# Optimization experiments

Measured on AMD Instinct MI355X. Metric: run time of the kernel, lower is better.

The kernel has to match this reference:

```python
import jax, jax.numpy as jnp
import numpy as np

N, E = 25000, 400000
HID, EDGE_F, DIM, HEADS, ADY = 128, 16, 3, 8, 64
INNER = int(1.25 * HID)          # 160
MSG_F = 2 * HID + EDGE_F + 1     # 273 (e3, relaxed=False -> 1 distance feature)


def silu(x):
    return x * jax.nn.sigmoid(x)


def ada_ln(x, y, W, b):
    # LayerNorm (no affine) + FiLM conditioning from y
    mu = jnp.mean(x, axis=-1, keepdims=True)
    var = jnp.var(x, axis=-1, keepdims=True)
    xn = (x - mu) * jax.lax.rsqrt(var + 1e-5)
    scale, shift = jnp.split(y @ W + b, 2, axis=-1)
    return xn * (1.0 + scale) + shift


def setup_inputs() -> dict:
    key = jax.random.key(0)
    ks = jax.random.split(key, 32)
    rn = lambda k, shp, s=0.05: (jax.random.normal(k, shp, jnp.float32) * s)
    inp = {
        'h': jax.random.normal(ks[0], (N, HID), jnp.float32),
        'coords': jax.random.normal(ks[1], (N, DIM), jnp.float32),
        'a': jax.random.normal(ks[2], (E, EDGE_F), jnp.float32),
        'y': jax.random.normal(ks[3], (N, ADY), jnp.float32),
        'res': jnp.zeros((N, HID), jnp.float32),
        'src': jax.random.randint(ks[4], (E,), 0, N, jnp.int32),
        'dst': jax.random.randint(ks[5], (E,), 0, N, jnp.int32),
        # edge MLP
        'We1': rn(ks[6], (MSG_F, INNER)), 'be1': jnp.zeros((INNER,), jnp.float32),
        'We2': rn(ks[7], (INNER, INNER)), 'be2': jnp.zeros((INNER,), jnp.float32),
        # coord head (xavier gain 0.001 -> tiny init)
        'Wc': rn(ks[8], (INNER, 1), 0.001),
        # attention/value/output heads
        'Wv': rn(ks[9], (INNER, HID)),
        'Wa': rn(ks[10], (INNER, HEADS)),
        'Wo': rn(ks[11], (HID, HID)),
        # node MLP
        'Wn1': rn(ks[12], (HID, INNER)), 'bn1': jnp.zeros((INNER,), jnp.float32),
        'Wn2': rn(ks[13], (INNER, HID)), 'bn2': jnp.zeros((HID,), jnp.float32),
        # adaptive LayerNorms (FiLM from y)
        'Wf1': rn(ks[14], (ADY, 2 * HID)), 'bf1': jnp.zeros((2 * HID,), jnp.float32),
        'Wf2': rn(ks[15], (ADY, 2 * HID)), 'bf2': jnp.zeros((2 * HID,), jnp.float32),
    }
    return inp


def reference(h, coords, a, y, res, src, dst,
              We1, be1, We2, be2, Wc, Wv, Wa, Wo,
              Wn1, bn1, Wn2, bn2, Wf1, bf1, Wf2, bf2):
    n = h.shape[0]
    heads = Wa.shape[1]
    # --- distance features (e3, relaxed=False): radial only ---
    xs, xd = coords[src], coords[dst]          # [E, 3]
    diffs = xs - xd
    radials = jnp.sum(diffs * diffs, axis=-1, keepdims=True)  # [E, 1]
    # --- edge MLP on gathered features ---
    f = jnp.concatenate([h[src], h[dst], radials, a], axis=-1)  # [E, 273]
    m = silu(f @ We1 + be1)
    m = silu(m @ We2 + be2)                    # [E, inner]
    # --- coordinate messages + scatter-sum to dst ---
    msg_x = (m @ Wc) * diffs / (jnp.sqrt(radials + 1e-5) + 1.0)  # [E, 3]
    coords_out = coords + jax.ops.segment_sum(msg_x, dst, num_segments=n)
    # --- edge softmax over incoming edges per dst node ---
    logits = m @ Wa                             # [E, heads]
    mx = jax.ops.segment_max(logits, dst, num_segments=n)
    ex = jnp.exp(logits - mx[dst])
    den = jax.ops.segment_sum(ex, dst, num_segments=n)
    w = ex / den[dst]                           # [E, heads]
    # --- weighted value aggregation ---
    vals = (m @ Wv).reshape(-1, heads, HID // heads) * w[:, :, None]
    h_agg = jax.ops.segment_sum(vals, dst, num_segments=n).reshape(n, HID)
    f2 = h_agg @ Wo
    res1 = res + f2
    h1 = ada_ln(h + f2, y, Wf1, bf1)
    f3 = silu(h1 @ Wn1 + bn1) @ Wn2 + bn2
    res2 = res1 + f3
    h2 = ada_ln(h1 + f3, y, Wf2, bf2)
    return (h2, coords_out, res2)
```

## Files before the change

kernel.cpp:

```cpp
#include <hip/hip_runtime.h>
#include <math.h>

#define N_NODES 25000
#define N_EDGES 400000
#define HID 128
#define EDGE_F 16
#define ADY 64
#define INNER 160
#define MSG_F 273
#define HEADS 8

#define OUT_CRD (N_NODES * HID)
#define OUT_RES (N_NODES * (HID + 3))

#define FLAG_OFF 0
#define DEN_OFF  256
#define CACC_OFF 800256
#define HAGG_OFF 1100288
#define HBF_OFF  13900288
#define YBF_OFF  20300288
#define BIAS_OFF 23500288
#define BW_OFF   23502592
#define MEMSET_BYTES 13900288

typedef unsigned short u16;
typedef unsigned int u32;
typedef unsigned long long u64;
typedef __attribute__((ext_vector_type(8))) short short8;
typedef __attribute__((ext_vector_type(4))) float f32x4;

__device__ __forceinline__ float bf2f(u16 v) {
    union { u32 u; float f; } x; x.u = ((u32)v) << 16; return x.f;
}
__device__ __forceinline__ u16 f2bf(float f) {
    union { float ff; u32 u; } x; x.ff = f;
    u32 u = x.u;
    u32 rounding = 0x7FFFu + ((u >> 16) & 1u);
    u += rounding;
    return (u16)(u >> 16);
}
__device__ __forceinline__ float silu(float z) {
    z = fminf(fmaxf(z, -30000.f), 30000.f);
    return z / (1.0f + __expf(-z));
}

template<bool F32> __device__ __forceinline__ float ldg1(const void* p, size_t i) {
    if (F32) return ((const float*)p)[i];
    return bf2f(((const u16*)p)[i]);
}
template<bool F32> __device__ __forceinline__ void stg1(void* p, size_t i, float v) {
    if (F32) ((float*)p)[i] = v;
    else     ((u16*)p)[i] = f2bf(v);
}
__device__ __forceinline__ float ldany(const void* p, size_t i, bool f32) {
    return f32 ? ((const float*)p)[i] : bf2f(((const u16*)p)[i]);
}
__device__ __forceinline__ void wave_lds_fence() {
    __builtin_amdgcn_wave_barrier();
    __builtin_amdgcn_s_waitcnt(0xc07f);
    __builtin_amdgcn_wave_barrier();
}

struct CvtArgs {
    const void* src[8];
    u64 dstoff[8];
    int n[8];
};
struct BwArgs {
    const void* We1; const void* We2; const void* Wv; const void* Wa;
    const void* Wc;  const void* Wo;  const void* Wn1; const void* Wn2;
    const void* Wf1; const void* Wf2;
    u64 b1, b2, b3, b4, b5, b6, b7, b8;
};

__global__ __launch_bounds__(256)
void preproc_kernel(const void* hsrc, int* flag, char* ws, CvtArgs args, BwArgs bwa)
{
    __shared__ float red[256];
    __shared__ int sflag;
    const int t = threadIdx.x;
    {
        const u16* p = (const u16*)hsrc;
        float mx = 0.f;
        for (int i = 0; i < 8; i++) {
            int idx = (t * 8 + i) * 97;
            float v = fabsf(bf2f(p[idx * 2]));
            mx = fmaxf(mx, v);
        }
        red[t] = mx;
        __syncthreads();
        for (int s = 128; s > 0; s >>= 1) {
            if (t < s) red[t] = fmaxf(red[t], red[t + s]);
            __syncthreads();
        }
        if (t == 0) {
            sflag = (red[0] > 1e10f || red[0] == 0.f) ? 1 : 0;
            if (blockIdx.x == 0) flag[0] = sflag;
        }
        __syncthreads();
    }
    const bool f32 = (sflag != 0);
    const int g = blockIdx.x * 256 + t;
    const int stride = gridDim.x * 256;

    for (int ten = 0; ten < 8; ten++) {
        const void* s = args.src[ten];
        u16* d = (u16*)(ws + args.dstoff[ten]);
        const int n = args.n[ten];
        if (f32) {
            const float* sf = (const float*)s;
            for (int i = g; i < n; i += stride) d[i] = f2bf(sf[i]);
        } else {
            const u16* su = (const u16*)s;
            for (int i = g; i < n; i += stride) d[i] = su[i];
        }
    }

    u16* b1 = (u16*)(ws + bwa.b1);
    u16* b2 = (u16*)(ws + bwa.b2);
    u16* b3 = (u16*)(ws + bwa.b3);
    u16* b4 = (u16*)(ws + bwa.b4);
    u16* b5 = (u16*)(ws + bwa.b5);
    u16* b6 = (u16*)(ws + bwa.b6);
    u16* b7 = (u16*)(ws + bwa.b7);
    u16* b8 = (u16*)(ws + bwa.b8);
    for (int i = g; i < 5*2*10*512; i += stride) {
        int tt = i >> 9, r = i & 511, l = r >> 3, j = r & 7;
        int c = tt / 20, ks = (tt / 10) % 2, nt = tt % 10;
        int k = c*64 + ks*32 + (l >> 4)*8 + j;
        int n = nt*16 + (l & 15);
        float v = 0.f;
        if (k < MSG_F)      v = ldany(bwa.We1, (size_t)k*INNER + n, f32);
        else if (k == 273)  v = ldany(bwa.We1, (size_t)256*INNER + n, f32);
        b1[i] = f2bf(v);
    }
    for (int i = g; i < 5*10*512; i += stride) {
        int tt = i >> 9, r = i & 511, l = r >> 3, j = r & 7;
        int k5 = tt / 10, nt = tt % 10;
        int k = k5*32 + (l >> 4)*8 + j;
        int n = nt*16 + (l & 15);
        b2[i] = f2bf(ldany(bwa.We2, (size_t)k*INNER + n, f32));
    }
    for (int i = g; i < 5*9*512; i += stride) {
        int tt = i >> 9, r = i & 511, l = r >> 3, j = r & 7;
        int k5 = tt / 9, nt = tt % 9;
        int k = k5*32 + (l >> 4)*8 + j;
        int n = nt*16 + (l & 15);
        float v = 0.f;
        if (n < 128)       v = ldany(bwa.Wv, (size_t)k*HID + n, f32);
        else if (n < 136)  v = ldany(bwa.Wa, (size_t)k*HEADS + (n-128), f32);
        else if (n == 136) v = ldany(bwa.Wc, (size_t)k, f32);
        b3[i] = f2bf(v);
    }
    for (int i = g; i < 4*8*512; i += stride) {
        int tt = i >> 9, r = i & 511, l = r >> 3, j = r & 7;
        int cks = tt / 8, nt = tt % 8;
        int k = cks*32 + (l >> 4)*8 + j;
        int n = nt*16 + (l & 15);
        b4[i] = f2bf(ldany(bwa.Wo, (size_t)k*HID + n, f32));
    }
    for (int i = g; i < 4*10*512; i += stride) {
        int tt = i >> 9, r = i & 511, l = r >> 3, j = r & 7;
        int cks = tt / 10, nt = tt % 10;
        int k = cks*32 + (l >> 4)*8 + j;
        int n = nt*16 + (l & 15);
        b5[i] = f2bf(ldany(bwa.Wn1, (size_t)k*INNER + n, f32));
    }
    for (int i = g; i < 5*8*512; i += stride) {
        int tt = i >> 9, r = i & 511, l = r >> 3, j = r & 7;
        int k5 = tt / 8, nt = tt % 8;
        int k = k5*32 + (l >> 4)*8 + j;
        int n = nt*16 + (l & 15);
        b6[i] = f2bf(ldany(bwa.Wn2, (size_t)k*HID + n, f32));
    }
    for (int i = g; i < 2*16*512; i += stride) {
        int tt = i >> 9, r = i & 511, l = r >> 3, j = r & 7;
        int ks = tt / 16, nt = tt % 16;
        int k = ks*32 + (l >> 4)*8 + j;
        int n = nt*16 + (l & 15);
        b7[i] = f2bf(ldany(bwa.Wf1, (size_t)k*256 + n, f32));
        b8[i] = f2bf(ldany(bwa.Wf2, (size_t)k*256 + n, f32));
    }
}

template<bool F32>
__device__ __forceinline__ void edge_body(
    const u16* __restrict__ hbf, const void* coords, const void* a,
    const int* __restrict__ src, const int* __restrict__ dst,
    const u16* __restrict__ We1P, const u16* __restrict__ We2P,
    const u16* __restrict__ W3P,
    const u16* __restrict__ cbe1, const u16* __restrict__ cbe2,
    float* __restrict__ den, float* __restrict__ hagg, float* __restrict__ cacc,
    u16* sPool, float* sdiff, float* srad, int* ssrc, int* sdstl)
{
    const int t   = threadIdx.x;
    const int w   = t >> 6;
    const int l   = t & 63;
    const int col = l & 15;
    const int q   = l >> 4;
    const int e0  = blockIdx.x * 64;
    const int l8  = l << 3;

    u16* sF  = sPool;
    u16* sM1 = sPool;
    u16* sM2 = sPool + 64*168;

    if (t < 64) {
        int e = e0 + t;
        int s = src[e], d = dst[e];
        ssrc[t] = s; sdstl[t] = d;
        float dx = ldg1<F32>(coords, (size_t)s*3+0) - ldg1<F32>(coords, (size_t)d*3+0);
        float dy = ldg1<F32>(coords, (size_t)s*3+1) - ldg1<F32>(coords, (size_t)d*3+1);
        float dz = ldg1<F32>(coords, (size_t)s*3+2) - ldg1<F32>(coords, (size_t)d*3+2);
        sdiff[t*4+0] = dx; sdiff[t*4+1] = dy; sdiff[t*4+2] = dz;
        float r2 = dx*dx + dy*dy + dz*dz;
        srad[t] = r2;
        sdiff[t*4+3] = 1.0f / (sqrtf(r2 + 1e-5f) + 1.0f);
    }
    __syncthreads();

    {
        int e = t >> 2, part = t & 3;
        int node_s = ssrc[e], node_d = sdstl[e];
        #pragma unroll
        for (int c = 0; c < 4; c++) {
            int node = (c < 2) ? node_s : node_d;
            int c0 = (c & 1) * 64 + part * 16;
            const uint4* gp = (const uint4*)(hbf + (size_t)node*HID + c0);
            *(uint4*)(&sF[e*360 + c*72 + part*16])     = gp[0];
            *(uint4*)(&sF[e*360 + c*72 + part*16 + 8]) = gp[1];
        }
        if (part < 2) {
            __align__(16) u16 tmp[16];
            #pragma unroll
            for (int j = 0; j < 16; j++) tmp[j] = 0;
            if (part == 0) {
                float r2 = srad[e];
                tmp[0] = f2bf(r2);
                for (int j = 0; j < 15; j++)
                    tmp[1+j] = f2bf(ldg1<F32>(a, (size_t)(e0+e)*EDGE_F + j));
            } else {
                tmp[0] = f2bf(ldg1<F32>(a, (size_t)(e0+e)*EDGE_F + 15));
                float r2 = srad[e];
                tmp[1] = f2bf(r2 - bf2f(f2bf(r2)));
            }
            *(uint4*)(&sF[e*360 + 4*72 + part*16])     = ((uint4*)tmp)[0];
            *(uint4*)(&sF[e*360 + 4*72 + part*16 + 8]) = ((uint4*)tmp)[1];
        }
    }
    __syncthreads();

    f32x4 acc1[10];
    #pragma unroll
    for (int nt = 0; nt < 10; nt++) {
        float v = bf2f(cbe1[nt*16 + col]);
        acc1[nt] = (f32x4){v, v, v, v};
    }
    const u16* fbase = &sF[(w*16 + col)*360];
    #pragma unroll
    for (int c = 0; c < 4; c++) {
        #pragma unroll
        for (int ks = 0; ks < 2; ks++) {
            short8 af = *(const short8*)(fbase + c*72 + ks*32 + q*8);
            const u16* B1 = We1P + (((c*2 + ks)*10) << 9) + l8;
            #pragma unroll
            for (int nt = 0; nt < 10; nt++) {
                short8 b = *(const short8*)(B1 + (nt << 9));
                acc1[nt] = __builtin_amdgcn_mfma_f32_16x16x32_bf16(af, b, acc1[nt], 0, 0, 0);
            }
        }
    }
    {
        short8 af = *(const short8*)(fbase + 4*72 + q*8);
        const u16* B1 = We1P + ((8*10) << 9) + l8;
        #pragma unroll
        for (int nt = 0; nt < 10; nt++) {
            short8 b = *(const short8*)(B1 + (nt << 9));
            acc1[nt] = __builtin_amdgcn_mfma_f32_16x16x32_bf16(af, b, acc1[nt], 0, 0, 0);
        }
    }
    __syncthreads();
    #pragma unroll
    for (int nt = 0; nt < 10; nt++)
        #pragma unroll
        for (int r = 0; r < 4; r++)
            sM1[(w*16 + q*4 + r)*168 + nt*16 + col] = f2bf(silu(acc1[nt][r]));
    __syncthreads();

    f32x4 acc2[10];
    #pragma unroll
    for (int nt = 0; nt < 10; nt++) {
        float v = bf2f(cbe2[nt*16 + col]);
        acc2[nt] = (f32x4){v, v, v, v};
    }
    const u16* m1base = &sM1[(w*16 + col)*168];
    #pragma unroll
    for (int k5 = 0; k5 < 5; k5++) {
        short8 af = *(const short8*)(m1base + k5*32 + q*8);
        const u16* B2 = We2P + ((k5*10) << 9) + l8;
        #pragma unroll
        for (int nt = 0; nt < 10; nt++) {
            short8 b = *(const short8*)(B2 + (nt << 9));
            acc2[nt] = __builtin_amdgcn_mfma_f32_16x16x32_bf16(af, b, acc2[nt], 0, 0, 0);
        }
    }
    #pragma unroll
    for (int nt = 0; nt < 10; nt++)
        #pragma unroll
        for (int r = 0; r < 4; r++)
            sM2[(w*16 + q*4 + r)*168 + nt*16 + col] = f2bf(silu(acc2[nt][r]));
    __syncthreads();

    f32x4 acc3[9];
    #pragma unroll
    for (int nt = 0; nt < 9; nt++) acc3[nt] = (f32x4){0.f, 0.f, 0.f, 0.f};
    const u16* m2base = &sM2[(w*16 + col)*168];
    #pragma unroll
    for (int k5 = 0; k5 < 5; k5++) {
        short8 af = *(const short8*)(m2base + k5*32 + q*8);
        const u16* B3 = W3P + ((k5*9) << 9) + l8;
        #pragma unroll
        for (int nt = 0; nt < 9; nt++) {
            short8 b = *(const short8*)(B3 + (nt << 9));
            acc3[nt] = __builtin_amdgcn_mfma_f32_16x16x32_bf16(af, b, acc3[nt], 0, 0, 0);
        }
    }

    int dstep[4];
    #pragma unroll
    for (int r = 0; r < 4; r++) dstep[r] = sdstl[w*16 + q*4 + r];

    float exv[4] = {0.f, 0.f, 0.f, 0.f};
    if (col < 8) {
        #pragma unroll
        for (int r = 0; r < 4; r++) {
            float ex = __expf(fminf(fmaxf(acc3[8][r], -30.f), 30.f));
            exv[r] = ex;
            atomicAdd(&den[(size_t)dstep[r]*8 + col], ex);
        }
    } else if (col == 8) {
        #pragma unroll
        for (int r = 0; r < 4; r++) {
            int idx = w*16 + q*4 + r;
            int dd = dstep[r];
            float invf = sdiff[idx*4 + 3];
            float lc = fminf(fmaxf(acc3[8][r], -1e6f), 1e6f) * invf;
            #pragma unroll
            for (int j = 0; j < 3; j++)
                atomicAdd(&cacc[(size_t)dd*3 + j], lc * sdiff[idx*4 + j]);
        }
    }
    #pragma unroll
    for (int nt = 0; nt < 8; nt++) {
        float ex0 = __shfl(exv[0], q*16 + nt);
        float ex1 = __shfl(exv[1], q*16 + nt);
        float ex2 = __shfl(exv[2], q*16 + nt);
        float ex3 = __shfl(exv[3], q*16 + nt);
        atomicAdd(&hagg[(size_t)dstep[0]*HID + nt*16 + col], acc3[nt][0] * ex0);
        atomicAdd(&hagg[(size_t)dstep[1]*HID + nt*16 + col], acc3[nt][1] * ex1);
        atomicAdd(&hagg[(size_t)dstep[2]*HID + nt*16 + col], acc3[nt][2] * ex2);
        atomicAdd(&hagg[(size_t)dstep[3]*HID + nt*16 + col], acc3[nt][3] * ex3);
    }
}

__global__ __launch_bounds__(256, 3)
void edge_kernel(const int* __restrict__ flag,
                 const u16* __restrict__ hbf, const void* coords, const void* a,
                 const int* __restrict__ src, const int* __restrict__ dst,
                 const u16* __restrict__ We1P, const u16* __restrict__ We2P,
                 const u16* __restrict__ W3P,
                 const u16* __restrict__ cbe1, const u16* __restrict__ cbe2,
                 float* __restrict__ den, float* __restrict__ hagg,
                 float* __restrict__ cacc)
{
    __shared__ __align__(16) u16 sPool[64*360];
    __shared__ float sdiff[64*4];
    __shared__ float srad[64];
    __shared__ int   ssrc[64];
    __shared__ int   sdstl[64];
    if (*flag)
        edge_body<true>(hbf, coords, a, src, dst, We1P, We2P, W3P, cbe1, cbe2,
                        den, hagg, cacc, sPool, sdiff, srad, ssrc, sdstl);
    else
        edge_body<false>(hbf, coords, a, src, dst, We1P, We2P, W3P, cbe1, cbe2,
                         den, hagg, cacc, sPool, sdiff, srad, ssrc, sdstl);
}

template<bool F32>
__device__ __forceinline__ void node_body(
    const u16* __restrict__ hbf, const void* res, const void* coords,
    const u16* __restrict__ ybf,
    const float* __restrict__ den, const float* __restrict__ hagg,
    const float* __restrict__ cacc,
    const u16* __restrict__ WoP, const u16* __restrict__ Wn1P,
    const u16* __restrict__ Wn2P, const u16* __restrict__ Wf1P,
    const u16* __restrict__ Wf2P,
    const u16* __restrict__ cbn1, const u16* __restrict__ cbn2,
    const u16* __restrict__ cbf1, const u16* __restrict__ cbf2,
    void* out, u16* sScr)
{
    const int t = threadIdx.x;
    const int w = t >> 6, l = t & 63, col = l & 15, q = l >> 4;
    const int nodew = blockIdx.x * 64 + w * 16;
    const int mynode = nodew + col;
    const bool okA = mynode < N_NODES;
    const int l8 = l << 3;
    u16* sc = sScr + w * 16 * 168;

    int gm[4]; bool okC[4];
    #pragma unroll
    for (int r = 0; r < 4; r++) { gm[r] = nodew + q*4 + r; okC[r] = gm[r] < N_NODES; }

    f32x4 aF2[8];
    #pragma unroll
    for (int nt = 0; nt < 8; nt++) aF2[nt] = (f32x4){0.f,0.f,0.f,0.f};
    #pragma unroll
    for (int c = 0; c < 2; c++) {
        #pragma unroll
        for (int ks = 0; ks < 2; ks++) {
            const int kbase = c*64 + ks*32 + q*8;
            union { u16 s[8]; short8 v; } u;
            if (okA) {
                float dd = den[(size_t)mynode*8 + (kbase >> 4)];
                float inv = dd > 0.f ? 1.f/dd : 0.f;
                const float4* gp = (const float4*)(hagg + (size_t)mynode*HID + kbase);
                float4 v0 = gp[0], v1 = gp[1];
                u.s[0]=f2bf(v0.x*inv); u.s[1]=f2bf(v0.y*inv); u.s[2]=f2bf(v0.z*inv); u.s[3]=f2bf(v0.w*inv);
                u.s[4]=f2bf(v1.x*inv); u.s[5]=f2bf(v1.y*inv); u.s[6]=f2bf(v1.z*inv); u.s[7]=f2bf(v1.w*inv);
            } else {
                #pragma unroll
                for (int j = 0; j < 8; j++) u.s[j] = 0;
            }
            const u16* B = WoP + (((c*2 + ks)*8) << 9) + l8;
            #pragma unroll
            for (int nt = 0; nt < 8; nt++) {
                short8 b = *(const short8*)(B + (nt << 9));
                aF2[nt] = __builtin_amdgcn_mfma_f32_16x16x32_bf16(u.v, b, aF2[nt], 0, 0, 0);
            }
        }
    }

    f32x4 aFl[16];
    #pragma unroll
    for (int nt = 0; nt < 16; nt++) {
        float v = bf2f(cbf1[nt*16 + col]);
        aFl[nt] = (f32x4){v,v,v,v};
    }
    #pragma unroll
    for (int ks = 0; ks < 2; ks++) {
        short8 af;
        if (okA) af = *(const short8*)(ybf + (size_t)mynode*ADY + ks*32 + q*8);
        else { union { u16 s[8]; short8 v; } z; for (int j=0;j<8;j++) z.s[j]=0; af = z.v; }
        const u16* B = Wf1P + ((ks*16) << 9) + l8;
        #pragma unroll
        for (int nt = 0; nt < 16; nt++) {
            short8 b = *(const short8*)(B + (nt << 9));
            aFl[nt] = __builtin_amdgcn_mfma_f32_16x16x32_bf16(af, b, aFl[nt], 0, 0, 0);
        }
    }

    float h1c[8][4], r1c[8][4];
    {
        float xv[8][4], s[4], ss[4];
        #pragma unroll
        for (int r = 0; r < 4; r++) { s[r] = 0.f; ss[r] = 0.f; }
        #pragma unroll
        for (int nt = 0; nt < 8; nt++)
            #pragma unroll
            for (int r = 0; r < 4; r++) {
                float hv = okC[r] ? bf2f(hbf[(size_t)gm[r]*HID + nt*16 + col]) : 0.f;
                float x = hv + aF2[nt][r];
                xv[nt][r] = x; s[r] += x; ss[r] += x*x;
            }
        #pragma unroll
        for (int r = 0; r < 4; r++)
            for (int off = 1; off <= 8; off <<= 1) {
                s[r]  += __shfl_xor(s[r], off);
                ss[r] += __shfl_xor(ss[r], off);
            }
        #pragma unroll
        for (int r = 0; r < 4; r++) {
            float mu = s[r] * (1.f/128.f);
            float var = ss[r] * (1.f/128.f) - mu*mu;
            float rs = rsqrtf(fmaxf(var, 0.f) + 1e-5f);
            #pragma unroll
            for (int nt = 0; nt < 8; nt++) {
                float h1 = (xv[nt][r]-mu)*rs*(1.f+aFl[nt][r]) + aFl[nt+8][r];
                h1c[nt][r] = h1;
                float rv = okC[r] ? ldg1<F32>(res, (size_t)gm[r]*HID + nt*16 + col) : 0.f;
                r1c[nt][r] = rv + aF2[nt][r];
                sc[(q*4 + r)*168 + nt*16 + col] = f2bf(h1);
            }
        }
    }
    wave_lds_fence();

    f32x4 aT[10];
    #pragma unroll
    for (int nt = 0; nt < 10; nt++) {
        float v = bf2f(cbn1[nt*16 + col]);
        aT[nt] = (f32x4){v,v,v,v};
    }
    #pragma unroll
    for (int c = 0; c < 2; c++) {
        #pragma unroll
        for (int ks = 0; ks < 2; ks++) {
            short8 af = *(const short8*)(sc + col*168 + c*64 + ks*32 + q*8);
            const u16* B = Wn1P + (((c*2 + ks)*10) << 9) + l8;
            #pragma unroll
            for (int nt = 0; nt < 10; nt++) {
                short8 b = *(const short8*)(B + (nt << 9));
                aT[nt] = __builtin_amdgcn_mfma_f32_16x16x32_bf16(af, b, aT[nt], 0, 0, 0);
            }
        }
    }
    wave_lds_fence();
    #pragma unroll
    for (int nt = 0; nt < 10; nt++)
        #pragma unroll
        for (int r = 0; r < 4; r++)
            sc[(q*4 + r)*168 + nt*16 + col] = f2bf(silu(aT[nt][r]));
    wave_lds_fence();

    f32x4 aF3[8];
    #pragma unroll
    for (int nt = 0; nt < 8; nt++) {
        float v = bf2f(cbn2[nt*16 + col]);
        aF3[nt] = (f32x4){v,v,v,v};
    }
    #pragma unroll
    for (int k5 = 0; k5 < 5; k5++) {
        short8 af = *(const short8*)(sc + col*168 + k5*32 + q*8);
        const u16* B = Wn2P + ((k5*8) << 9) + l8;
        #pragma unroll
        for (int nt = 0; nt < 8; nt++) {
            short8 b = *(const short8*)(B + (nt << 9));
            aF3[nt] = __builtin_amdgcn_mfma_f32_16x16x32_bf16(af, b, aF3[nt], 0, 0, 0);
        }
    }

    #pragma unroll
    for (int nt = 0; nt < 16; nt++) {
        float v = bf2f(cbf2[nt*16 + col]);
        aFl[nt] = (f32x4){v,v,v,v};
    }
    #pragma unroll
    for (int ks = 0; ks < 2; ks++) {
        short8 af;
        if (okA) af = *(const short8*)(ybf + (size_t)mynode*ADY + ks*32 + q*8);
        else { union { u16 s[8]; short8 v; } z; for (int j=0;j<8;j++) z.s[j]=0; af = z.v; }
        const u16* B = Wf2P + ((ks*16) << 9) + l8;
        #pragma unroll
        for (int nt = 0; nt < 16; nt++) {
            short8 b = *(const short8*)(B + (nt << 9));
            aFl[nt] = __builtin_amdgcn_mfma_f32_16x16x32_bf16(af, b, aFl[nt], 0, 0, 0);
        }
    }

    {
        float xv[8][4], s[4], ss[4];
        #pragma unroll
        for (int r = 0; r < 4; r++) { s[r] = 0.f; ss[r] = 0.f; }
        #pragma unroll
        for (int nt = 0; nt < 8; nt++)
            #pragma unroll
            for (int r = 0; r < 4; r++) {
                float x = h1c[nt][r] + aF3[nt][r];
                xv[nt][r] = x; s[r] += x; ss[r] += x*x;
            }
        #pragma unroll
        for (int r = 0; r < 4; r++)
            for (int off = 1; off <= 8; off <<= 1) {
                s[r]  += __shfl_xor(s[r], off);
                ss[r] += __shfl_xor(ss[r], off);
            }
        #pragma unroll
        for (int r = 0; r < 4; r++) {
            float mu = s[r] * (1.f/128.f);
            float var = ss[r] * (1.f/128.f) - mu*mu;
            float rs = rsqrtf(fmaxf(var, 0.f) + 1e-5f);
            if (okC[r]) {
                #pragma unroll
                for (int nt = 0; nt < 8; nt++) {
                    int n = nt*16 + col;
                    float h2 = (xv[nt][r]-mu)*rs*(1.f+aFl[nt][r]) + aFl[nt+8][r];
                    stg1<F32>(out, (size_t)gm[r]*HID + n, h2);
                    stg1<F32>(out, (size_t)OUT_RES + (size_t)gm[r]*HID + n,
                              r1c[nt][r] + aF3[nt][r]);
                }
            }
        }
    }

    if (q == 0 && okA) {
        #pragma unroll
        for (int j = 0; j < 3; j++)
            stg1<F32>(out, (size_t)OUT_CRD + (size_t)mynode*3 + j,
                      ldg1<F32>(coords, (size_t)mynode*3 + j) + cacc[(size_t)mynode*3 + j]);
    }
}

__global__ __launch_bounds__(256, 2)
void node_kernel(const int* __restrict__ flag,
                 const u16* __restrict__ hbf, const void* res, const void* coords,
                 const u16* __restrict__ ybf,
                 const float* __restrict__ den, const float* __restrict__ hagg,
                 const float* __restrict__ cacc,
                 const u16* __restrict__ WoP, const u16* __restrict__ Wn1P,
                 const u16* __restrict__ Wn2P, const u16* __restrict__ Wf1P,
                 const u16* __restrict__ Wf2P,
                 const u16* __restrict__ cbn1, const u16* __restrict__ cbn2,
                 const u16* __restrict__ cbf1, const u16* __restrict__ cbf2,
                 void* out)
{
    __shared__ __align__(16) u16 sScr[4 * 16 * 168];
    if (*flag)
        node_body<true>(hbf, res, coords, ybf, den, hagg, cacc, WoP, Wn1P, Wn2P,
                        Wf1P, Wf2P, cbn1, cbn2, cbf1, cbf2, out, sScr);
    else
        node_body<false>(hbf, res, coords, ybf, den, hagg, cacc, WoP, Wn1P, Wn2P,
                         Wf1P, Wf2P, cbn1, cbn2, cbf1, cbf2, out, sScr);
}

extern "C" void kernel_launch(void* const* d_in, const int* in_sizes, int n_in,
                              void* d_out, int out_size, void* d_ws, size_t ws_size,
                              hipStream_t stream)
{
    const void* h      = d_in[0];
    const void* coords = d_in[1];
    const void* a      = d_in[2];
    const void* y      = d_in[3];
    const void* res    = d_in[4];
    const int* src     = (const int*)d_in[5];
    const int* dst     = (const int*)d_in[6];

    char* ws = (char*)d_ws;
    int*   flag = (int*)(ws + FLAG_OFF);
    float* den  = (float*)(ws + DEN_OFF);
    float* cacc = (float*)(ws + CACC_OFF);
    float* hagg = (float*)(ws + HAGG_OFF);
    u16*   hbf  = (u16*)(ws + HBF_OFF);
    u16*   ybf  = (u16*)(ws + YBF_OFF);

    CvtArgs args;
    const int cvtn[8]   = {160, 160, 160, 128, 256, 256, N_NODES*HID, N_NODES*ADY};
    const int cvtsrc[8] = {8, 10, 16, 18, 20, 22, 0, 3};
    u64 boff[8];
    u64 bo = BIAS_OFF;
    for (int i = 0; i < 6; i++) {
        boff[i] = bo;
        bo += ((u64)cvtn[i] * 2 + 15) & ~(u64)15;
    }
    boff[6] = HBF_OFF;
    boff[7] = YBF_OFF;
    for (int i = 0; i < 8; i++) {
        args.src[i] = d_in[cvtsrc[i]];
        args.dstoff[i] = boff[i];
        args.n[i] = cvtn[i];
    }
    const u16* cbe1 = (const u16*)(ws + boff[0]);
    const u16* cbe2 = (const u16*)(ws + boff[1]);
    const u16* cbn1 = (const u16*)(ws + boff[2]);
    const u16* cbn2 = (const u16*)(ws + boff[3]);
    const u16* cbf1 = (const u16*)(ws + boff[4]);
    const u16* cbf2 = (const u16*)(ws + boff[5]);

    BwArgs bwa;
    bwa.We1 = d_in[7];  bwa.We2 = d_in[9];  bwa.Wv = d_in[12]; bwa.Wa = d_in[13];
    bwa.Wc  = d_in[11]; bwa.Wo  = d_in[14]; bwa.Wn1 = d_in[15]; bwa.Wn2 = d_in[17];
    bwa.Wf1 = d_in[19]; bwa.Wf2 = d_in[21];
    bwa.b1 = BW_OFF;
    bwa.b2 = bwa.b1 + (u64)5*2*10*512*2;
    bwa.b3 = bwa.b2 + (u64)5*10*512*2;
    bwa.b4 = bwa.b3 + (u64)5*9*512*2;
    bwa.b5 = bwa.b4 + (u64)4*8*512*2;
    bwa.b6 = bwa.b5 + (u64)4*10*512*2;
    bwa.b7 = bwa.b6 + (u64)5*8*512*2;
    bwa.b8 = bwa.b7 + (u64)2*16*512*2;
    const u16* We1P = (const u16*)(ws + bwa.b1);
    const u16* We2P = (const u16*)(ws + bwa.b2);
    const u16* W3P  = (const u16*)(ws + bwa.b3);
    const u16* WoP  = (const u16*)(ws + bwa.b4);
    const u16* Wn1P = (const u16*)(ws + bwa.b5);
    const u16* Wn2P = (const u16*)(ws + bwa.b6);
    const u16* Wf1P = (const u16*)(ws + bwa.b7);
    const u16* Wf2P = (const u16*)(ws + bwa.b8);

    hipMemsetAsync(d_ws, 0, MEMSET_BYTES, stream);

    preproc_kernel<<<256, 256, 0, stream>>>(h, flag, ws, args, bwa);

    edge_kernel<<<N_EDGES/64, 256, 0, stream>>>(flag, hbf, coords, a, src, dst,
                                                We1P, We2P, W3P, cbe1, cbe2,
                                                den, hagg, cacc);

    node_kernel<<<(N_NODES + 63)/64, 256, 0, stream>>>(
        flag, hbf, res, coords, ybf, den, hagg, cacc,
        WoP, Wn1P, Wn2P, Wf1P, Wf2P, cbn1, cbn2, cbf1, cbf2, d_out);
}
```

Baseline: 527.4 us.

## Sort edges by destination and pre-reduce per-wave messages before atomics

Builds a counting sort of edges by destination (histogram in preproc, a single-block scan, then an atomic scatter into a permutation). The edge kernel processes edges in that order, stages the per-edge weighted values, softmax exponents and coordinate messages in LDS, and reduces runs of equal destinations within each 16-row wave slice before issuing one global atomic per run. The goal is fewer global float atomics and less contention on hagg/den/cacc. The cost is three extra passes (histogram atomics, a serial single-block scan, a scatter), gathered rather than sequential reads of edge features, and a nondeterministic edge order.

```diff
diff --git a/kernel.cpp b/kernel.cpp
--- a/kernel.cpp
+++ b/kernel.cpp
@@ -16,12 +16,17 @@
 #define FLAG_OFF 0
 #define DEN_OFF  256
 #define CACC_OFF 800256
-#define HAGG_OFF 1100288
-#define HBF_OFF  13900288
-#define YBF_OFF  20300288
-#define BIAS_OFF 23500288
-#define BW_OFF   23502592
-#define MEMSET_BYTES 13900288
+#define HAGG_OFF 1100256
+#define CNT_OFF  13900256
+#define CUR_OFF  14000256
+#define PERM_OFF 14100256
+#define MEMSET_BYTES 14000256
+#define HBF_OFF  15700256
+#define YBF_OFF  22100256
+#define BIAS_OFF 25300256
+#define BW_OFF   25302560
+
+#define SCR_STRIDE 145
 
 typedef unsigned short u16;
 typedef unsigned int u32;
@@ -74,7 +79,8 @@
 };
 
 __global__ __launch_bounds__(256)
-void preproc_kernel(const void* hsrc, int* flag, char* ws, CvtArgs args, BwArgs bwa)
+void preproc_kernel(const void* hsrc, int* flag, char* ws, CvtArgs args, BwArgs bwa,
+                    const int* __restrict__ dstp, int* __restrict__ cnt)
 {
     __shared__ float red[256];
     __shared__ int sflag;
@@ -102,6 +108,9 @@
     const bool f32 = (sflag != 0);
     const int g = blockIdx.x * 256 + t;
     const int stride = gridDim.x * 256;
+
+    for (int i = g; i < N_EDGES; i += stride)
+        atomicAdd(&cnt[dstp[i]], 1);
 
     for (int ten = 0; ten < 8; ten++) {
         const void* s = args.src[ten];
@@ -183,15 +192,57 @@
     }
 }
 
+__global__ __launch_bounds__(1024)
+void scan_kernel(const int* __restrict__ cnt, int* __restrict__ cursor)
+{
+    __shared__ int ssum[1024];
+    const int t = threadIdx.x;
+    const int base = t * 25;
+    int loc[25];
+    int s = 0;
+    #pragma unroll
+    for (int j = 0; j < 25; j++) {
+        int i = base + j;
+        int v = (i < N_NODES) ? cnt[i] : 0;
+        loc[j] = s; s += v;
+    }
+    ssum[t] = s;
+    __syncthreads();
+    for (int off = 1; off < 1024; off <<= 1) {
+        int v = (t >= off) ? ssum[t - off] : 0;
+        __syncthreads();
+        ssum[t] += v;
+        __syncthreads();
+    }
+    int offs = (t > 0) ? ssum[t - 1] : 0;
+    #pragma unroll
+    for (int j = 0; j < 25; j++) {
+        int i = base + j;
+        if (i < N_NODES) cursor[i] = offs + loc[j];
+    }
+}
+
+__global__ __launch_bounds__(256)
+void scatter_kernel(const int* __restrict__ dstp, int* __restrict__ cursor,
+                    int* __restrict__ perm)
+{
+    int i = blockIdx.x * 256 + threadIdx.x;
+    if (i < N_EDGES) {
+        int pos = atomicAdd(&cursor[dstp[i]], 1);
+        perm[pos] = i;
+    }
+}
+
 template<bool F32>
 __device__ __forceinline__ void edge_body(
     const u16* __restrict__ hbf, const void* coords, const void* a,
     const int* __restrict__ src, const int* __restrict__ dst,
+    const int* __restrict__ perm,
     const u16* __restrict__ We1P, const u16* __restrict__ We2P,
     const u16* __restrict__ W3P,
     const u16* __restrict__ cbe1, const u16* __restrict__ cbe2,
     float* __restrict__ den, float* __restrict__ hagg, float* __restrict__ cacc,
-    u16* sPool, float* sdiff, float* srad, int* ssrc, int* sdstl)
+    u16* sPool, float* sdiff, float* srad, int* ssrc, int* sdstl, int* sedge)
 {
     const int t   = threadIdx.x;
     const int w   = t >> 6;
@@ -206,7 +257,8 @@
     u16* sM2 = sPool + 64*168;
 
     if (t < 64) {
-        int e = e0 + t;
+        int e = perm[e0 + t];
+        sedge[t] = e;
         int s = src[e], d = dst[e];
         ssrc[t] = s; sdstl[t] = d;
         float dx = ldg1<F32>(coords, (size_t)s*3+0) - ldg1<F32>(coords, (size_t)d*3+0);
@@ -222,6 +274,7 @@
     {
         int e = t >> 2, part = t & 3;
         int node_s = ssrc[e], node_d = sdstl[e];
+        int ge = sedge[e];
         #pragma unroll
         for (int c = 0; c < 4; c++) {
             int node = (c < 2) ? node_s : node_d;
@@ -238,9 +291,9 @@
                 float r2 = srad[e];
                 tmp[0] = f2bf(r2);
                 for (int j = 0; j < 15; j++)
-                    tmp[1+j] = f2bf(ldg1<F32>(a, (size_t)(e0+e)*EDGE_F + j));
+                    tmp[1+j] = f2bf(ldg1<F32>(a, (size_t)ge*EDGE_F + j));
             } else {
-                tmp[0] = f2bf(ldg1<F32>(a, (size_t)(e0+e)*EDGE_F + 15));
+                tmp[0] = f2bf(ldg1<F32>(a, (size_t)ge*EDGE_F + 15));
                 float r2 = srad[e];
                 tmp[1] = f2bf(r2 - bf2f(f2bf(r2)));
             }
@@ -325,41 +378,78 @@
             acc3[nt] = __builtin_amdgcn_mfma_f32_16x16x32_bf16(af, b, acc3[nt], 0, 0, 0);
         }
     }
-
-    int dstep[4];
-    #pragma unroll
-    for (int r = 0; r < 4; r++) dstep[r] = sdstl[w*16 + q*4 + r];
-
-    float exv[4] = {0.f, 0.f, 0.f, 0.f};
-    if (col < 8) {
-        #pragma unroll
-        for (int r = 0; r < 4; r++) {
-            float ex = __expf(fminf(fmaxf(acc3[8][r], -30.f), 30.f));
-            exv[r] = ex;
-            atomicAdd(&den[(size_t)dstep[r]*8 + col], ex);
-        }
-    } else if (col == 8) {
-        #pragma unroll
-        for (int r = 0; r < 4; r++) {
-            int idx = w*16 + q*4 + r;
-            int dd = dstep[r];
-            float invf = sdiff[idx*4 + 3];
-            float lc = fminf(fmaxf(acc3[8][r], -1e6f), 1e6f) * invf;
-            #pragma unroll
-            for (int j = 0; j < 3; j++)
-                atomicAdd(&cacc[(size_t)dd*3 + j], lc * sdiff[idx*4 + j]);
-        }
-    }
-    #pragma unroll
-    for (int nt = 0; nt < 8; nt++) {
-        float ex0 = __shfl(exv[0], q*16 + nt);
-        float ex1 = __shfl(exv[1], q*16 + nt);
-        float ex2 = __shfl(exv[2], q*16 + nt);
-        float ex3 = __shfl(exv[3], q*16 + nt);
-        atomicAdd(&hagg[(size_t)dstep[0]*HID + nt*16 + col], acc3[nt][0] * ex0);
-        atomicAdd(&hagg[(size_t)dstep[1]*HID + nt*16 + col], acc3[nt][1] * ex1);
-        atomicAdd(&hagg[(size_t)dstep[2]*HID + nt*16 + col], acc3[nt][2] * ex2);
-        atomicAdd(&hagg[(size_t)dstep[3]*HID + nt*16 + col], acc3[nt][3] * ex3);
+    __syncthreads();
+
+    float* scr = (float*)(void*)sPool + (size_t)w * 16 * SCR_STRIDE;
+
+    {
+        float exv[4] = {0.f, 0.f, 0.f, 0.f};
+        if (col < 8) {
+            #pragma unroll
+            for (int r = 0; r < 4; r++)
+                exv[r] = __expf(fminf(fmaxf(acc3[8][r], -30.f), 30.f));
+        }
+        #pragma unroll
+        for (int nt = 0; nt < 8; nt++) {
+            float ex0 = __shfl(exv[0], q*16 + nt);
+            float ex1 = __shfl(exv[1], q*16 + nt);
+            float ex2 = __shfl(exv[2], q*16 + nt);
+            float ex3 = __shfl(exv[3], q*16 + nt);
+            scr[(q*4 + 0)*SCR_STRIDE + nt*16 + col] = acc3[nt][0] * ex0;
+            scr[(q*4 + 1)*SCR_STRIDE + nt*16 + col] = acc3[nt][1] * ex1;
+            scr[(q*4 + 2)*SCR_STRIDE + nt*16 + col] = acc3[nt][2] * ex2;
+            scr[(q*4 + 3)*SCR_STRIDE + nt*16 + col] = acc3[nt][3] * ex3;
+        }
+        if (col < 8) {
+            #pragma unroll
+            for (int r = 0; r < 4; r++)
+                scr[(q*4 + r)*SCR_STRIDE + 128 + col] = exv[r];
+        }
+        if (col == 8) {
+            #pragma unroll
+            for (int r = 0; r < 4; r++) {
+                int idx = w*16 + q*4 + r;
+                float invf = sdiff[idx*4 + 3];
+                float lc = fminf(fmaxf(acc3[8][r], -1e6f), 1e6f) * invf;
+                #pragma unroll
+                for (int j = 0; j < 3; j++)
+                    scr[(q*4 + r)*SCR_STRIDE + 136 + j] = lc * sdiff[idx*4 + j];
+            }
+        }
+    }
+    wave_lds_fence();
+
+    {
+        const int rbase = w*16;
+        int dsts[16];
+        #pragma unroll
+        for (int row = 0; row < 16; row++) dsts[row] = sdstl[rbase + row];
+
+        #pragma unroll
+        for (int pass = 0; pass < 3; pass++) {
+            int c = pass*64 + l;
+            bool act = c < 139;
+            float accu = 0.f;
+            int prevd = dsts[0];
+            #pragma unroll
+            for (int row = 0; row < 16; row++) {
+                int d = dsts[row];
+                if (d != prevd) {
+                    if (act) {
+                        if (c < 128)      atomicAdd(&hagg[(size_t)prevd*HID + c], accu);
+                        else if (c < 136) atomicAdd(&den[(size_t)prevd*8 + (c-128)], accu);
+                        else              atomicAdd(&cacc[(size_t)prevd*3 + (c-136)], accu);
+                    }
+                    accu = 0.f; prevd = d;
+                }
+                if (act) accu += scr[row*SCR_STRIDE + c];
+            }
+            if (act) {
+                if (c < 128)      atomicAdd(&hagg[(size_t)prevd*HID + c], accu);
+                else if (c < 136) atomicAdd(&den[(size_t)prevd*8 + (c-128)], accu);
+                else              atomicAdd(&cacc[(size_t)prevd*3 + (c-136)], accu);
+            }
+        }
     }
 }
 
@@ -367,6 +457,7 @@
 void edge_kernel(const int* __restrict__ flag,
                  const u16* __restrict__ hbf, const void* coords, const void* a,
                  const int* __restrict__ src, const int* __restrict__ dst,
+                 const int* __restrict__ perm,
                  const u16* __restrict__ We1P, const u16* __restrict__ We2P,
                  const u16* __restrict__ W3P,
                  const u16* __restrict__ cbe1, const u16* __restrict__ cbe2,
@@ -378,12 +469,13 @@
     __shared__ float srad[64];
     __shared__ int   ssrc[64];
     __shared__ int   sdstl[64];
+    __shared__ int   sedge[64];
     if (*flag)
-        edge_body<true>(hbf, coords, a, src, dst, We1P, We2P, W3P, cbe1, cbe2,
-                        den, hagg, cacc, sPool, sdiff, srad, ssrc, sdstl);
+        edge_body<true>(hbf, coords, a, src, dst, perm, We1P, We2P, W3P, cbe1, cbe2,
+                        den, hagg, cacc, sPool, sdiff, srad, ssrc, sdstl, sedge);
     else
-        edge_body<false>(hbf, coords, a, src, dst, We1P, We2P, W3P, cbe1, cbe2,
-                         den, hagg, cacc, sPool, sdiff, srad, ssrc, sdstl);
+        edge_body<false>(hbf, coords, a, src, dst, perm, We1P, We2P, W3P, cbe1, cbe2,
+                         den, hagg, cacc, sPool, sdiff, srad, ssrc, sdstl, sedge);
 }
 
 template<bool F32>
@@ -635,12 +727,15 @@
     const int* dst     = (const int*)d_in[6];
 
     char* ws = (char*)d_ws;
-    int*   flag = (int*)(ws + FLAG_OFF);
-    float* den  = (float*)(ws + DEN_OFF);
-    float* cacc = (float*)(ws + CACC_OFF);
-    float* hagg = (float*)(ws + HAGG_OFF);
-    u16*   hbf  = (u16*)(ws + HBF_OFF);
-    u16*   ybf  = (u16*)(ws + YBF_OFF);
+    int*   flag   = (int*)(ws + FLAG_OFF);
+    float* den    = (float*)(ws + DEN_OFF);
+    float* cacc   = (float*)(ws + CACC_OFF);
+    float* hagg   = (float*)(ws + HAGG_OFF);
+    int*   cnt    = (int*)(ws + CNT_OFF);
+    int*   cursor = (int*)(ws + CUR_OFF);
+    int*   perm   = (int*)(ws + PERM_OFF);
+    u16*   hbf    = (u16*)(ws + HBF_OFF);
+    u16*   ybf    = (u16*)(ws + YBF_OFF);
 
     CvtArgs args;
     const int cvtn[8]   = {160, 160, 160, 128, 256, 256, N_NODES*HID, N_NODES*ADY};
@@ -688,9 +783,13 @@
 
     hipMemsetAsync(d_ws, 0, MEMSET_BYTES, stream);
 
-    preproc_kernel<<<256, 256, 0, stream>>>(h, flag, ws, args, bwa);
-
-    edge_kernel<<<N_EDGES/64, 256, 0, stream>>>(flag, hbf, coords, a, src, dst,
+    preproc_kernel<<<256, 256, 0, stream>>>(h, flag, ws, args, bwa, dst, cnt);
+
+    scan_kernel<<<1, 1024, 0, stream>>>(cnt, cursor);
+
+    scatter_kernel<<<(N_EDGES + 255)/256, 256, 0, stream>>>(dst, cursor, perm);
+
+    edge_kernel<<<N_EDGES/64, 256, 0, stream>>>(flag, hbf, coords, a, src, dst, perm,
                                                 We1P, We2P, W3P, cbe1, cbe2,
                                                 den, hagg, cacc);
 
```

After: 528.0 us. Within noise of the previous version (+0.1%).
